# Kernel optimization log

Measured on AMD Instinct MI355X. Metric: run time of the kernel, lower is better.

The kernel has to match this reference:

```python
import jax, jax.numpy as jnp
import numpy as np

N_ENTITY = 64368
N_REL = 12
DIM = 128
NB = 8
N_ITEM = 6924
E = 1_000_000
B = 128
L = 32


def setup_inputs() -> dict:
    key = jax.random.key(0)
    ks = jax.random.split(key, 12)
    return {
        "edge_idx": jax.random.randint(ks[0], (2, E), 0, N_ENTITY),
        "edge_type": jax.random.randint(ks[1], (E,), 0, N_REL),
        "seed_ids": jax.random.randint(ks[2], (B, L), 0, N_ITEM),
        "seed_len": jax.random.randint(ks[3], (B,), 0, L + 1),
        "labels": jax.random.randint(ks[4], (B,), 0, N_ITEM),
        # RGCN basis-decomposition params (x=None => in_channels = n_entity)
        "basis": jax.random.normal(ks[5], (NB, N_ENTITY, DIM), dtype=jnp.float32) * 0.02,
        "att": jax.random.normal(ks[6], (N_REL, NB), dtype=jnp.float32) * 0.1,
        "root": jax.random.normal(ks[7], (N_ENTITY, DIM), dtype=jnp.float32) * 0.02,
        "rgcn_bias": jnp.zeros((DIM,), dtype=jnp.float32),
        # SelfAttentionLayer params
        "attn_a": jax.random.normal(ks[8], (DIM, DIM), dtype=jnp.float32) * 0.1,
        "attn_b": jax.random.normal(ks[9], (DIM, 1), dtype=jnp.float32) * 0.1,
        # output linear bias (weight is tied to item node features per F.linear(u, nodes, bias))
        "out_bias": jnp.zeros((N_ITEM,), dtype=jnp.float32),
    }


def _rgcn(edge_idx, edge_type, basis, att, root, rgcn_bias):
    src, dst = edge_idx[0], edge_idx[1]
    # composed per-relation weight acting as relation-specific node embeddings: [R, N, D]
    w = jnp.einsum('rb,bnd->rnd', att, basis)
    msg = w[edge_type, src]  # [E, D] relation-indexed gather
    aggr = jax.ops.segment_sum(msg, dst, num_segments=N_ENTITY)
    deg = jax.ops.segment_sum(jnp.ones((msg.shape[0],), msg.dtype), dst, num_segments=N_ENTITY)
    aggr = aggr / jnp.maximum(deg, 1.0)[:, None]  # mean aggregation
    return aggr + root + rgcn_bias  # update: aggr + root (x=None) + bias


def _pool(nodes, seed_ids, seed_len, attn_a, attn_b):
    h = nodes[seed_ids]  # [B, L, D] ragged gather (padded)
    e = (jnp.tanh(h @ attn_a) @ attn_b)[..., 0]  # [B, L]
    mask = jnp.arange(seed_ids.shape[1])[None, :] < seed_len[:, None]
    attn = jax.nn.softmax(jnp.where(mask, e, -1e9), axis=-1)
    u = jnp.einsum('bl,bld->bd', attn, h)
    return jnp.where((seed_len > 0)[:, None], u, 0.0)  # empty seed set -> zeros


def reference(edge_idx, edge_type, seed_ids, seed_len, labels,
              basis, att, root, rgcn_bias, attn_a, attn_b, out_bias):
    nodes = _rgcn(edge_idx, edge_type, basis, att, root, rgcn_bias)  # [N, D]
    u = _pool(nodes, seed_ids, seed_len, attn_a, attn_b)             # [B, D]
    scores = u @ nodes[:N_ITEM].T + out_bias                          # [B, N_ITEM]
    return scores
```

## Files before the change

kernel.cpp:

```cpp
#include <hip/hip_runtime.h>
#include <math.h>

#define N_ENTITY 64368
#define N_REL 12
#define DIM 128
#define NB 8
#define N_ITEM 6924
#define NEDGE 1000000
#define BATCH 128
#define SEQL 32
#define ITEM_TILE 32

__global__ __launch_bounds__(256) void edge_scatter_kernel(
    const int* __restrict__ e_src, const int* __restrict__ e_dst,
    const int* __restrict__ e_type, const float* __restrict__ basis,
    const float* __restrict__ att, float* __restrict__ aggr,
    float* __restrict__ deg)
{
    __shared__ float att_s[N_REL * NB];
    if (threadIdx.x < N_REL * NB) att_s[threadIdx.x] = att[threadIdx.x];
    __syncthreads();

    int gid  = blockIdx.x * 256 + threadIdx.x;
    int lane = threadIdx.x & 63;

    int d = 0, s = 0, t = 0;
    bool keep = false;
    if (gid < NEDGE) {
        d = e_dst[gid];
        keep = (d < N_ITEM);
        if (keep) { s = e_src[gid]; t = e_type[gid]; }
    }
    unsigned long long mask = __ballot(keep);
    while (mask) {
        int l = __ffsll((unsigned long long)mask) - 1;
        mask &= mask - 1;
        int dd = __shfl(d, l);
        int ss = __shfl(s, l);
        int tt = __shfl(t, l);

        const float* bp = basis + (size_t)ss * DIM + lane * 2;
        float accx = 0.f, accy = 0.f;
        #pragma unroll
        for (int b = 0; b < NB; ++b) {
            float a = att_s[tt * NB + b];
            float2 v = *reinterpret_cast<const float2*>(bp + (size_t)b * N_ENTITY * DIM);
            accx += a * v.x;
            accy += a * v.y;
        }
        float* outp = aggr + (size_t)dd * DIM + lane * 2;
        atomicAdd(outp,     accx);
        atomicAdd(outp + 1, accy);
        if (lane == 0) atomicAdd(deg + dd, 1.0f);
    }
}

__global__ __launch_bounds__(256) void finalize_kernel(
    const float* __restrict__ aggr, const float* __restrict__ deg,
    const float* __restrict__ root, const float* __restrict__ bias,
    float* __restrict__ nodes)
{
    int idx = blockIdx.x * 256 + threadIdx.x;
    if (idx >= N_ITEM * (DIM / 4)) return;
    int n  = idx >> 5;
    int kq = idx & 31;
    float inv = 1.0f / fmaxf(deg[n], 1.0f);
    float4 a  = reinterpret_cast<const float4*>(aggr)[idx];
    float4 r  = reinterpret_cast<const float4*>(root)[idx];
    float4 bs = reinterpret_cast<const float4*>(bias)[kq];
    float4 o;
    o.x = a.x * inv + r.x + bs.x;
    o.y = a.y * inv + r.y + bs.y;
    o.z = a.z * inv + r.z + bs.z;
    o.w = a.w * inv + r.w + bs.w;
    reinterpret_cast<float4*>(nodes)[idx] = o;
}

__global__ __launch_bounds__(256) void pool_kernel(
    const float* __restrict__ nodes, const int* __restrict__ seed_ids,
    const int* __restrict__ seed_len, const float* __restrict__ attn_a,
    const float* __restrict__ attn_b, float* __restrict__ u)
{
    __shared__ float h[SEQL * 132];
    __shared__ float ev[SEQL];
    __shared__ float attw[SEQL];
    __shared__ int   seeds[SEQL];

    int b   = blockIdx.x;
    int tid = threadIdx.x;
    int len = seed_len[b];

    if (tid < SEQL) seeds[tid] = seed_ids[b * SEQL + tid];
    __syncthreads();

    for (int idx = tid; idx < SEQL * (DIM / 4); idx += 256) {
        int l  = idx >> 5;
        int kq = idx & 31;
        float4 v = reinterpret_cast<const float4*>(nodes)[(size_t)seeds[l] * 32 + kq];
        *reinterpret_cast<float4*>(h + l * 132 + kq * 4) = v;
    }
    __syncthreads();

    {
        int l = tid >> 3;
        int j = tid & 7;
        float dot[16];
        #pragma unroll
        for (int i = 0; i < 16; ++i) dot[i] = 0.f;
        const float* hr = h + l * 132;
        for (int k = 0; k < DIM; ++k) {
            float hv = hr[k];
            const float4* ar = reinterpret_cast<const float4*>(attn_a + k * DIM + j * 16);
            float4 a0 = ar[0], a1 = ar[1], a2 = ar[2], a3 = ar[3];
            dot[0]  += hv * a0.x; dot[1]  += hv * a0.y; dot[2]  += hv * a0.z; dot[3]  += hv * a0.w;
            dot[4]  += hv * a1.x; dot[5]  += hv * a1.y; dot[6]  += hv * a1.z; dot[7]  += hv * a1.w;
            dot[8]  += hv * a2.x; dot[9]  += hv * a2.y; dot[10] += hv * a2.z; dot[11] += hv * a2.w;
            dot[12] += hv * a3.x; dot[13] += hv * a3.y; dot[14] += hv * a3.z; dot[15] += hv * a3.w;
        }
        float sum = 0.f;
        #pragma unroll
        for (int i = 0; i < 16; ++i) sum += tanhf(dot[i]) * attn_b[j * 16 + i];
        sum += __shfl_xor(sum, 1);
        sum += __shfl_xor(sum, 2);
        sum += __shfl_xor(sum, 4);
        if (j == 0) ev[l] = sum;
    }
    __syncthreads();

    if (tid < SEQL) {
        float val = (tid < len) ? ev[tid] : -3.0e38f;
        float m = val;
        #pragma unroll
        for (int off = 16; off > 0; off >>= 1) m = fmaxf(m, __shfl_xor(m, off));
        float p = (tid < len) ? expf(val - m) : 0.f;
        float ssum = p;
        #pragma unroll
        for (int off = 16; off > 0; off >>= 1) ssum += __shfl_xor(ssum, off);
        attw[tid] = (len > 0) ? p / ssum : 0.f;
    }
    __syncthreads();

    if (tid < DIM) {
        float acc = 0.f;
        #pragma unroll
        for (int l = 0; l < SEQL; ++l) acc += attw[l] * h[l * 132 + tid];
        u[(size_t)b * DIM + tid] = acc;
    }
}

__global__ __launch_bounds__(256) void score_kernel(
    const float* __restrict__ nodes, const float* __restrict__ u,
    const float* __restrict__ out_bias, float* __restrict__ out)
{
    __shared__ float us[BATCH * DIM];
    __shared__ float ns[ITEM_TILE * 132];
    int tid   = threadIdx.x;
    int item0 = blockIdx.x * ITEM_TILE;

    for (int idx = tid; idx < BATCH * (DIM / 4); idx += 256)
        reinterpret_cast<float4*>(us)[idx] = reinterpret_cast<const float4*>(u)[idx];

    for (int idx = tid; idx < ITEM_TILE * (DIM / 4); idx += 256) {
        int j  = idx >> 5;
        int kq = idx & 31;
        int item = item0 + j;
        float4 v = make_float4(0.f, 0.f, 0.f, 0.f);
        if (item < N_ITEM) v = reinterpret_cast<const float4*>(nodes)[(size_t)item * 32 + kq];
        *reinterpret_cast<float4*>(ns + j * 132 + kq * 4) = v;
    }
    __syncthreads();

    int jg = tid & 15;
    int bg = tid >> 4;
    float acc0[8], acc1[8];
    #pragma unroll
    for (int i = 0; i < 8; ++i) { acc0[i] = 0.f; acc1[i] = 0.f; }
    const float* n0p = ns + (jg * 2 + 0) * 132;
    const float* n1p = ns + (jg * 2 + 1) * 132;
    for (int k = 0; k < DIM; k += 4) {
        float4 n0 = *reinterpret_cast<const float4*>(n0p + k);
        float4 n1 = *reinterpret_cast<const float4*>(n1p + k);
        #pragma unroll
        for (int bb = 0; bb < 8; ++bb) {
            float4 uv = *reinterpret_cast<const float4*>(us + (bg * 8 + bb) * DIM + k);
            acc0[bb] += uv.x * n0.x + uv.y * n0.y + uv.z * n0.z + uv.w * n0.w;
            acc1[bb] += uv.x * n1.x + uv.y * n1.y + uv.z * n1.z + uv.w * n1.w;
        }
    }
    #pragma unroll
    for (int bb = 0; bb < 8; ++bb) {
        int bi  = bg * 8 + bb;
        int it0 = item0 + jg * 2;
        if (it0     < N_ITEM) out[(size_t)bi * N_ITEM + it0]     = acc0[bb] + out_bias[it0];
        if (it0 + 1 < N_ITEM) out[(size_t)bi * N_ITEM + it0 + 1] = acc1[bb] + out_bias[it0 + 1];
    }
}

extern "C" void kernel_launch(void* const* d_in, const int* in_sizes, int n_in,
                              void* d_out, int out_size, void* d_ws, size_t ws_size,
                              hipStream_t stream)
{
    const int*   e_src     = (const int*)d_in[0];
    const int*   e_dst     = e_src + NEDGE;
    const int*   e_type    = (const int*)d_in[1];
    const int*   seed_ids  = (const int*)d_in[2];
    const int*   seed_len  = (const int*)d_in[3];
    const float* basis     = (const float*)d_in[5];
    const float* att       = (const float*)d_in[6];
    const float* root      = (const float*)d_in[7];
    const float* rgcn_bias = (const float*)d_in[8];
    const float* attn_a    = (const float*)d_in[9];
    const float* attn_b    = (const float*)d_in[10];
    const float* out_bias  = (const float*)d_in[11];
    float*       out       = (float*)d_out;

    float* aggr  = (float*)d_ws;
    float* deg   = aggr + (size_t)N_ITEM * DIM;
    float* nodes = deg + N_ITEM;
    float* u     = nodes + (size_t)N_ITEM * DIM;

    hipMemsetAsync(aggr, 0, ((size_t)N_ITEM * DIM + N_ITEM) * sizeof(float), stream);

    edge_scatter_kernel<<<(NEDGE + 255) / 256, 256, 0, stream>>>(
        e_src, e_dst, e_type, basis, att, aggr, deg);
    finalize_kernel<<<(N_ITEM * (DIM / 4) + 255) / 256, 256, 0, stream>>>(
        aggr, deg, root, rgcn_bias, nodes);
    pool_kernel<<<BATCH, 256, 0, stream>>>(
        nodes, seed_ids, seed_len, attn_a, attn_b, u);
    score_kernel<<<(N_ITEM + ITEM_TILE - 1) / ITEM_TILE, 256, 0, stream>>>(
        nodes, u, out_bias, out);
}
```

Before: 486.3 us.

## Replace atomic edge scatter with CSR bucket sort and per-row gather aggregation

```diff
diff --git a/kernel.cpp b/kernel.cpp
--- a/kernel.cpp
+++ b/kernel.cpp
@@ -11,69 +11,106 @@
 #define SEQL 32
 #define ITEM_TILE 32
 
-__global__ __launch_bounds__(256) void edge_scatter_kernel(
+__global__ __launch_bounds__(256) void count_kernel(
+    const int* __restrict__ e_dst, int* __restrict__ cnt)
+{
+    int gid = blockIdx.x * 256 + threadIdx.x;
+    if (gid < NEDGE) {
+        int d = e_dst[gid];
+        if (d < N_ITEM) atomicAdd(&cnt[d], 1);
+    }
+}
+
+#define SCAN_CHUNK 28
+__global__ __launch_bounds__(256) void scan_kernel(
+    const int* __restrict__ cnt, int* __restrict__ offs, int* __restrict__ cursor)
+{
+    __shared__ int part[256];
+    int tid = threadIdx.x;
+    int local[SCAN_CHUNK];
+    int s = 0;
+    #pragma unroll
+    for (int i = 0; i < SCAN_CHUNK; ++i) {
+        int idx = tid * SCAN_CHUNK + i;
+        local[i] = s;
+        s += (idx < N_ITEM) ? cnt[idx] : 0;
+    }
+    part[tid] = s;
+    __syncthreads();
+    for (int off = 1; off < 256; off <<= 1) {
+        int v = (tid >= off) ? part[tid - off] : 0;
+        __syncthreads();
+        part[tid] += v;
+        __syncthreads();
+    }
+    int base = (tid == 0) ? 0 : part[tid - 1];
+    #pragma unroll
+    for (int i = 0; i < SCAN_CHUNK; ++i) {
+        int idx = tid * SCAN_CHUNK + i;
+        if (idx < N_ITEM) { int o = base + local[i]; offs[idx] = o; cursor[idx] = o; }
+    }
+    if (tid == 255) offs[N_ITEM] = part[255];
+}
+
+__global__ __launch_bounds__(256) void fill_kernel(
     const int* __restrict__ e_src, const int* __restrict__ e_dst,
-    const int* __restrict__ e_type, const float* __restrict__ basis,
-    const float* __restrict__ att, float* __restrict__ aggr,
-    float* __restrict__ deg)
+    const int* __restrict__ e_type, int* __restrict__ cursor,
+    int* __restrict__ bucket)
+{
+    int gid = blockIdx.x * 256 + threadIdx.x;
+    if (gid < NEDGE) {
+        int d = e_dst[gid];
+        if (d < N_ITEM) {
+            int pos = atomicAdd(&cursor[d], 1);
+            bucket[pos] = e_src[gid] | (e_type[gid] << 17);
+        }
+    }
+}
+
+__global__ __launch_bounds__(256) void aggregate_kernel(
+    const int* __restrict__ offs, const int* __restrict__ bucket,
+    const float* __restrict__ basis, const float* __restrict__ att,
+    const float* __restrict__ root, const float* __restrict__ bias,
+    float* __restrict__ nodes)
 {
     __shared__ float att_s[N_REL * NB];
     if (threadIdx.x < N_REL * NB) att_s[threadIdx.x] = att[threadIdx.x];
     __syncthreads();
 
-    int gid  = blockIdx.x * 256 + threadIdx.x;
+    int wave = threadIdx.x >> 6;
     int lane = threadIdx.x & 63;
-
-    int d = 0, s = 0, t = 0;
-    bool keep = false;
-    if (gid < NEDGE) {
-        d = e_dst[gid];
-        keep = (d < N_ITEM);
-        if (keep) { s = e_src[gid]; t = e_type[gid]; }
-    }
-    unsigned long long mask = __ballot(keep);
-    while (mask) {
-        int l = __ffsll((unsigned long long)mask) - 1;
-        mask &= mask - 1;
-        int dd = __shfl(d, l);
-        int ss = __shfl(s, l);
-        int tt = __shfl(t, l);
-
-        const float* bp = basis + (size_t)ss * DIM + lane * 2;
-        float accx = 0.f, accy = 0.f;
-        #pragma unroll
-        for (int b = 0; b < NB; ++b) {
-            float a = att_s[tt * NB + b];
-            float2 v = *reinterpret_cast<const float2*>(bp + (size_t)b * N_ENTITY * DIM);
-            accx += a * v.x;
-            accy += a * v.y;
-        }
-        float* outp = aggr + (size_t)dd * DIM + lane * 2;
-        atomicAdd(outp,     accx);
-        atomicAdd(outp + 1, accy);
-        if (lane == 0) atomicAdd(deg + dd, 1.0f);
-    }
-}
-
-__global__ __launch_bounds__(256) void finalize_kernel(
-    const float* __restrict__ aggr, const float* __restrict__ deg,
-    const float* __restrict__ root, const float* __restrict__ bias,
-    float* __restrict__ nodes)
-{
-    int idx = blockIdx.x * 256 + threadIdx.x;
-    if (idx >= N_ITEM * (DIM / 4)) return;
-    int n  = idx >> 5;
-    int kq = idx & 31;
-    float inv = 1.0f / fmaxf(deg[n], 1.0f);
-    float4 a  = reinterpret_cast<const float4*>(aggr)[idx];
-    float4 r  = reinterpret_cast<const float4*>(root)[idx];
-    float4 bs = reinterpret_cast<const float4*>(bias)[kq];
-    float4 o;
-    o.x = a.x * inv + r.x + bs.x;
-    o.y = a.y * inv + r.y + bs.y;
-    o.z = a.z * inv + r.z + bs.z;
-    o.w = a.w * inv + r.w + bs.w;
-    reinterpret_cast<float4*>(nodes)[idx] = o;
+    int row  = blockIdx.x * 4 + wave;
+    if (row >= N_ITEM) return;
+
+    int o0 = offs[row], o1 = offs[row + 1];
+    int n  = o1 - o0;
+
+    float accx = 0.f, accy = 0.f;
+    for (int base = 0; base < n; base += 64) {
+        int m = n - base; if (m > 64) m = 64;
+        int pk = 0;
+        if (lane < m) pk = bucket[o0 + base + lane];
+        for (int j = 0; j < m; ++j) {
+            int p  = __shfl(pk, j);
+            int ss = p & 0x1FFFF;
+            int tt = p >> 17;
+            const float* bp = basis + (size_t)ss * DIM + lane * 2;
+            #pragma unroll
+            for (int b = 0; b < NB; ++b) {
+                float a = att_s[tt * NB + b];
+                float2 v = *reinterpret_cast<const float2*>(bp + (size_t)b * (N_ENTITY * DIM));
+                accx += a * v.x;
+                accy += a * v.y;
+            }
+        }
+    }
+    float inv = 1.0f / fmaxf((float)n, 1.0f);
+    float2 r  = *reinterpret_cast<const float2*>(root + (size_t)row * DIM + lane * 2);
+    float2 bs = *reinterpret_cast<const float2*>(bias + lane * 2);
+    float2 o;
+    o.x = accx * inv + r.x + bs.x;
+    o.y = accy * inv + r.y + bs.y;
+    *reinterpret_cast<float2*>(nodes + (size_t)row * DIM + lane * 2) = o;
 }
 
 __global__ __launch_bounds__(256) void pool_kernel(
@@ -214,17 +251,20 @@
     const float* out_bias  = (const float*)d_in[11];
     float*       out       = (float*)d_out;
 
-    float* aggr  = (float*)d_ws;
-    float* deg   = aggr + (size_t)N_ITEM * DIM;
-    float* nodes = deg + N_ITEM;
-    float* u     = nodes + (size_t)N_ITEM * DIM;
-
-    hipMemsetAsync(aggr, 0, ((size_t)N_ITEM * DIM + N_ITEM) * sizeof(float), stream);
-
-    edge_scatter_kernel<<<(NEDGE + 255) / 256, 256, 0, stream>>>(
-        e_src, e_dst, e_type, basis, att, aggr, deg);
-    finalize_kernel<<<(N_ITEM * (DIM / 4) + 255) / 256, 256, 0, stream>>>(
-        aggr, deg, root, rgcn_bias, nodes);
+    int*   cnt    = (int*)d_ws;
+    int*   offs   = cnt + 6928;
+    int*   cursor = offs + 6928;
+    int*   bucket = cursor + 6928;
+    float* nodes  = (float*)(bucket + NEDGE);
+    float* u      = nodes + (size_t)N_ITEM * DIM;
+
+    hipMemsetAsync(cnt, 0, 6928 * sizeof(int), stream);
+
+    count_kernel<<<(NEDGE + 255) / 256, 256, 0, stream>>>(e_dst, cnt);
+    scan_kernel<<<1, 256, 0, stream>>>(cnt, offs, cursor);
+    fill_kernel<<<(NEDGE + 255) / 256, 256, 0, stream>>>(e_src, e_dst, e_type, cursor, bucket);
+    aggregate_kernel<<<(N_ITEM + 3) / 4, 256, 0, stream>>>(
+        offs, bucket, basis, att, root, rgcn_bias, nodes);
     pool_kernel<<<BATCH, 256, 0, stream>>>(
         nodes, seed_ids, seed_len, attn_a, attn_b, u);
     score_kernel<<<(N_ITEM + ITEM_TILE - 1) / ITEM_TILE, 256, 0, stream>>>(
```

Measured after the change: 481.1 us. No clear change (-1.1%).

## Bucket edges by source node to reuse basis rows across edges

Applied to the files above, without the earlier changes.

```diff
diff --git a/kernel.cpp b/kernel.cpp
--- a/kernel.cpp
+++ b/kernel.cpp
@@ -11,47 +11,103 @@
 #define SEQL 32
 #define ITEM_TILE 32
 
-__global__ __launch_bounds__(256) void edge_scatter_kernel(
+#define CNT_PAD 64384
+#define OFFS_PAD 64400
+
+__global__ __launch_bounds__(256) void count_kernel(
     const int* __restrict__ e_src, const int* __restrict__ e_dst,
-    const int* __restrict__ e_type, const float* __restrict__ basis,
-    const float* __restrict__ att, float* __restrict__ aggr,
-    float* __restrict__ deg)
+    int* __restrict__ cnt)
+{
+    int gid = blockIdx.x * 256 + threadIdx.x;
+    if (gid < NEDGE) {
+        if (e_dst[gid] < N_ITEM) atomicAdd(&cnt[e_src[gid]], 1);
+    }
+}
+
+#define SCAN_C 63
+__global__ __launch_bounds__(1024) void scan_kernel(
+    const int* __restrict__ cnt, int* __restrict__ offs, int* __restrict__ cursor)
+{
+    __shared__ int part[1024];
+    int tid = threadIdx.x;
+    int s = 0;
+    for (int i = 0; i < SCAN_C; ++i) {
+        int idx = tid * SCAN_C + i;
+        s += (idx < N_ENTITY) ? cnt[idx] : 0;
+    }
+    part[tid] = s;
+    __syncthreads();
+    for (int off = 1; off < 1024; off <<= 1) {
+        int v = (tid >= off) ? part[tid - off] : 0;
+        __syncthreads();
+        part[tid] += v;
+        __syncthreads();
+    }
+    int run = (tid == 0) ? 0 : part[tid - 1];
+    for (int i = 0; i < SCAN_C; ++i) {
+        int idx = tid * SCAN_C + i;
+        if (idx < N_ENTITY) {
+            offs[idx] = run; cursor[idx] = run;
+            run += cnt[idx];
+        }
+    }
+    if (tid == 1023) offs[N_ENTITY] = part[1023];
+}
+
+__global__ __launch_bounds__(256) void fill_kernel(
+    const int* __restrict__ e_src, const int* __restrict__ e_dst,
+    const int* __restrict__ e_type, int* __restrict__ cursor,
+    int* __restrict__ bucket, float* __restrict__ deg)
+{
+    int gid = blockIdx.x * 256 + threadIdx.x;
+    if (gid < NEDGE) {
+        int d = e_dst[gid];
+        if (d < N_ITEM) {
+            int s = e_src[gid];
+            int pos = atomicAdd(&cursor[s], 1);
+            bucket[pos] = d | (e_type[gid] << 13);
+            atomicAdd(&deg[d], 1.0f);
+        }
+    }
+}
+
+__global__ __launch_bounds__(256) void aggregate_kernel(
+    const int* __restrict__ offs, const int* __restrict__ bucket,
+    const float* __restrict__ basis, const float* __restrict__ att,
+    float* __restrict__ aggr)
 {
     __shared__ float att_s[N_REL * NB];
     if (threadIdx.x < N_REL * NB) att_s[threadIdx.x] = att[threadIdx.x];
     __syncthreads();
 
-    int gid  = blockIdx.x * 256 + threadIdx.x;
+    int wave = threadIdx.x >> 6;
     int lane = threadIdx.x & 63;
-
-    int d = 0, s = 0, t = 0;
-    bool keep = false;
-    if (gid < NEDGE) {
-        d = e_dst[gid];
-        keep = (d < N_ITEM);
-        if (keep) { s = e_src[gid]; t = e_type[gid]; }
-    }
-    unsigned long long mask = __ballot(keep);
-    while (mask) {
-        int l = __ffsll((unsigned long long)mask) - 1;
-        mask &= mask - 1;
-        int dd = __shfl(d, l);
-        int ss = __shfl(s, l);
-        int tt = __shfl(t, l);
-
-        const float* bp = basis + (size_t)ss * DIM + lane * 2;
-        float accx = 0.f, accy = 0.f;
+    int src  = blockIdx.x * 4 + wave;
+    if (src >= N_ENTITY) return;
+
+    int o0 = offs[src], o1 = offs[src + 1];
+    if (o0 == o1) return;
+
+    const float* bp = basis + (size_t)src * DIM + lane * 2;
+    float2 row[NB];
+    #pragma unroll
+    for (int b = 0; b < NB; ++b)
+        row[b] = *reinterpret_cast<const float2*>(bp + (size_t)b * (N_ENTITY * DIM));
+
+    for (int j = o0; j < o1; ++j) {
+        int p = bucket[j];
+        int d = p & 8191;
+        int t = p >> 13;
+        float mx = 0.f, my = 0.f;
         #pragma unroll
         for (int b = 0; b < NB; ++b) {
-            float a = att_s[tt * NB + b];
-            float2 v = *reinterpret_cast<const float2*>(bp + (size_t)b * N_ENTITY * DIM);
-            accx += a * v.x;
-            accy += a * v.y;
-        }
-        float* outp = aggr + (size_t)dd * DIM + lane * 2;
-        atomicAdd(outp,     accx);
-        atomicAdd(outp + 1, accy);
-        if (lane == 0) atomicAdd(deg + dd, 1.0f);
+            float a = att_s[t * NB + b];
+            mx += a * row[b].x;
+            my += a * row[b].y;
+        }
+        float* outp = aggr + (size_t)d * DIM + lane * 2;
+        atomicAdd(outp,     mx);
+        atomicAdd(outp + 1, my);
     }
 }
 
@@ -214,15 +270,23 @@
     const float* out_bias  = (const float*)d_in[11];
     float*       out       = (float*)d_out;
 
-    float* aggr  = (float*)d_ws;
-    float* deg   = aggr + (size_t)N_ITEM * DIM;
-    float* nodes = deg + N_ITEM;
-    float* u     = nodes + (size_t)N_ITEM * DIM;
-
-    hipMemsetAsync(aggr, 0, ((size_t)N_ITEM * DIM + N_ITEM) * sizeof(float), stream);
-
-    edge_scatter_kernel<<<(NEDGE + 255) / 256, 256, 0, stream>>>(
-        e_src, e_dst, e_type, basis, att, aggr, deg);
+    int*   cnt    = (int*)d_ws;
+    float* aggr   = (float*)(cnt + CNT_PAD);
+    float* deg    = aggr + (size_t)N_ITEM * DIM;
+    int*   offs   = (int*)(deg + 6928);
+    int*   cursor = offs + OFFS_PAD;
+    int*   bucket = cursor + OFFS_PAD;
+    float* nodes  = (float*)(bucket + NEDGE);
+    float* u      = nodes + (size_t)N_ITEM * DIM;
+
+    hipMemsetAsync(cnt, 0, (CNT_PAD + (size_t)N_ITEM * DIM + 6928) * sizeof(int), stream);
+
+    count_kernel<<<(NEDGE + 255) / 256, 256, 0, stream>>>(e_src, e_dst, cnt);
+    scan_kernel<<<1, 1024, 0, stream>>>(cnt, offs, cursor);
+    fill_kernel<<<(NEDGE + 255) / 256, 256, 0, stream>>>(
+        e_src, e_dst, e_type, cursor, bucket, deg);
+    aggregate_kernel<<<(N_ENTITY + 3) / 4, 256, 0, stream>>>(
+        offs, bucket, basis, att, aggr);
     finalize_kernel<<<(N_ITEM * (DIM / 4) + 255) / 256, 256, 0, stream>>>(
         aggr, deg, root, rgcn_bias, nodes);
     pool_kernel<<<BATCH, 256, 0, stream>>>(
```

Result: slower. 632.4 us (+30.0%).
